# Performance work log

Measured on AMD Instinct MI355X. Metric: run time of the kernel, lower is better.

The kernel has to match this reference:

```python
import jax, jax.numpy as jnp
import numpy as np

FP8_MAX = 448.0  # torch.finfo(float8_e4m3fn).max
BLK = 128
EPS = 1e-12

def fp8_round(x):
    # saturated cast to float8_e4m3fn and back (emulates to_fp8_saturated)
    y = jnp.clip(x, -FP8_MAX, FP8_MAX)
    return y.astype(jnp.float8_e4m3fn).astype(jnp.float32)

def per_tile_quant_dequant(x):
    # activation: 1x128 tiles along the feature dim
    S, D = x.shape
    t = x.reshape(S, D // BLK, BLK)
    amax = jnp.max(jnp.abs(t), axis=-1, keepdims=True)
    scale = jnp.maximum(amax, EPS) / FP8_MAX
    q = fp8_round(t / scale)
    return (q * scale).reshape(S, D)

def per_block_quant_dequant_weight(w):
    # weight: 128x128 blocks, w is [ne, dout, din]
    ne, do, di = w.shape
    blk = w.reshape(ne, do // BLK, BLK, di // BLK, BLK)
    amax = jnp.max(jnp.abs(blk), axis=(2, 4), keepdims=True)
    scale = jnp.maximum(amax, EPS) / FP8_MAX
    q = fp8_round(blk / scale)
    return (q * scale).reshape(ne, do, di)

def setup_inputs() -> dict:
    key = jax.random.key(0)
    k1, k2 = jax.random.split(key)
    NE, DOUT, DIN, SEQ = 8, 1024, 2048, 16384
    x = jax.random.normal(k1, (SEQ, DIN), dtype=jnp.float32)
    w = jax.random.normal(k2, (NE * DOUT, DIN), dtype=jnp.float32) * 0.02
    tokens_per_expert = jnp.full((NE,), SEQ // NE, dtype=jnp.int32)
    return {"input": x, "tokens_per_expert": tokens_per_expert, "weight": w}

def reference(input, tokens_per_expert, weight):
    NE = tokens_per_expert.shape[0]
    S, DIN = input.shape
    DOUT = weight.shape[0] // NE
    w = weight.reshape(NE, DOUT, DIN)
    w_dq = per_block_quant_dequant_weight(w)   # fp8 per-block weight, dequantized
    x_dq = per_tile_quant_dequant(input)       # fp8 per-tile activation, dequantized
    # grouped varlen GEMM; tokens are split equally across experts here
    T = S // NE
    xe = x_dq.reshape(NE, T, DIN)
    out = jnp.einsum('etd,eod->eto', xe, w_dq)  # [ne, T, dout]
    return out.reshape(S, DOUT)
```

## Files before the change

### kernel.cpp

```cpp
#include <hip/hip_runtime.h>
#include <hip/hip_bf16.h>
#include <hip/hip_fp8.h>

#define SEQ   16384
#define DIN_  2048
#define DOUT_ 1024
#define NE_   8
#define TPE   (SEQ / NE_)
#define NT    (DIN_ / 64)

typedef __bf16 bf16x8 __attribute__((ext_vector_type(8)));
typedef __bf16 bf16x4 __attribute__((ext_vector_type(4)));
typedef float  f32x4  __attribute__((ext_vector_type(4)));

#define GLD(gp, lp) __builtin_amdgcn_global_load_lds( \
    (const __attribute__((address_space(1))) unsigned int*)(gp), \
    (__attribute__((address_space(3))) unsigned int*)(lp), 16, 0, 0)

__device__ __forceinline__ float fp8_round_dq_m(float v, float sinv, float s) {
    float r = v * sinv;
    r = fminf(fmaxf(r, -448.0f), 448.0f);
    __hip_fp8_e4m3 q(r);
    return (float)q * s;
}

__global__ __launch_bounds__(256) void quant_x_kernel(const float* __restrict__ X,
                                                      __bf16* __restrict__ Xq) {
    const int t    = threadIdx.x;
    const int lane = t & 63;
    const int wave = t >> 6;
    const int tile = wave * 4 + (lane >> 4);
    const int sub  = lane & 15;
    const size_t off = (size_t)tile * 128 + sub * 8;

    const int row0 = blockIdx.x * 4;
    float4 v0[4], v1[4];
    float mx[4];
    #pragma unroll
    for (int r = 0; r < 4; ++r) {
        const float* p = X + (size_t)(row0 + r) * DIN_ + off;
        v0[r] = *(const float4*)p;
        v1[r] = *(const float4*)(p + 4);
        mx[r] = fmaxf(fmaxf(fmaxf(fabsf(v0[r].x), fabsf(v0[r].y)),
                            fmaxf(fabsf(v0[r].z), fabsf(v0[r].w))),
                      fmaxf(fmaxf(fabsf(v1[r].x), fabsf(v1[r].y)),
                            fmaxf(fabsf(v1[r].z), fabsf(v1[r].w))));
    }
    #pragma unroll
    for (int o = 1; o < 16; o <<= 1) {
        #pragma unroll
        for (int r = 0; r < 4; ++r)
            mx[r] = fmaxf(mx[r], __shfl_xor(mx[r], o, 64));
    }
    #pragma unroll
    for (int r = 0; r < 4; ++r) {
        const float s    = fmaxf(mx[r], 1e-12f) / 448.0f;
        const float sinv = 1.0f / s;
        bf16x8 o;
        o[0] = (__bf16)fp8_round_dq_m(v0[r].x, sinv, s);
        o[1] = (__bf16)fp8_round_dq_m(v0[r].y, sinv, s);
        o[2] = (__bf16)fp8_round_dq_m(v0[r].z, sinv, s);
        o[3] = (__bf16)fp8_round_dq_m(v0[r].w, sinv, s);
        o[4] = (__bf16)fp8_round_dq_m(v1[r].x, sinv, s);
        o[5] = (__bf16)fp8_round_dq_m(v1[r].y, sinv, s);
        o[6] = (__bf16)fp8_round_dq_m(v1[r].z, sinv, s);
        o[7] = (__bf16)fp8_round_dq_m(v1[r].w, sinv, s);
        *(bf16x8*)(Xq + (size_t)(row0 + r) * DIN_ + off) = o;
    }
}

__global__ __launch_bounds__(256) void quant_w_kernel(const float* __restrict__ W,
                                                      __bf16* __restrict__ Wq) {
    const int rb = blockIdx.x >> 4;
    const int cb = blockIdx.x & 15;
    const int t  = threadIdx.x;

    const float* base = W + (size_t)(rb * 128) * DIN_ + cb * 128;
    const int r0 = t >> 5;
    const int c0 = (t & 31) * 4;

    float4 v[16];
    float m = 0.0f;
    #pragma unroll
    for (int i = 0; i < 16; ++i) {
        v[i] = *(const float4*)(base + (size_t)(i * 8 + r0) * DIN_ + c0);
        m = fmaxf(m, fmaxf(fmaxf(fabsf(v[i].x), fabsf(v[i].y)),
                           fmaxf(fabsf(v[i].z), fabsf(v[i].w))));
    }
    #pragma unroll
    for (int off = 1; off < 64; off <<= 1)
        m = fmaxf(m, __shfl_xor(m, off, 64));
    __shared__ float smx[4];
    if ((t & 63) == 0) smx[t >> 6] = m;
    __syncthreads();
    const float amax = fmaxf(fmaxf(smx[0], smx[1]), fmaxf(smx[2], smx[3]));
    const float s    = fmaxf(amax, 1e-12f) / 448.0f;
    const float sinv = 1.0f / s;

    __bf16* obase = Wq + (size_t)(rb * 128) * DIN_ + cb * 128;
    #pragma unroll
    for (int i = 0; i < 16; ++i) {
        bf16x4 o;
        o[0] = (__bf16)fp8_round_dq_m(v[i].x, sinv, s);
        o[1] = (__bf16)fp8_round_dq_m(v[i].y, sinv, s);
        o[2] = (__bf16)fp8_round_dq_m(v[i].z, sinv, s);
        o[3] = (__bf16)fp8_round_dq_m(v[i].w, sinv, s);
        *(bf16x4*)(obase + (size_t)(i * 8 + r0) * DIN_ + c0) = o;
    }
}

__global__ __launch_bounds__(512, 2) void gemm_kernel(const __bf16* __restrict__ X,
                                                      const __bf16* __restrict__ W,
                                                      float* __restrict__ out) {
    __shared__ __align__(16) unsigned char lds[131072];

    const int bid  = blockIdx.x;
    const int wgid = (bid & 7) * 32 + (bid >> 3);
    const int e    = wgid >> 5;
    const int tile = wgid & 31;
    const int brow = tile >> 2;
    const int bcol = tile & 3;

    const int t     = threadIdx.x;
    const int lane  = t & 63;
    const int wave  = t >> 6;
    const int wm    = wave >> 2;
    const int wn    = wave & 3;
    const int flane = lane & 15;

    const __bf16* Xt = X + (size_t)(e * TPE + brow * 256) * DIN_;
    const __bf16* Wt = W + (size_t)(e * DOUT_ + bcol * 256) * DIN_;

    auto stage = [&](int j, bool isA) {
        if (j >= NT) return;
        const unsigned base = (isA ? 0u : 65536u) + (unsigned)(j & 1) * 32768u;
        const __bf16* src = isA ? Xt : Wt;
        #pragma unroll
        for (int i = 0; i < 4; ++i) {
            const unsigned p = (unsigned)i * 8192u + (unsigned)t * 16u;
            const unsigned q = p ^ (((p >> 7) & 7u) << 4);
            GLD(src + (size_t)(q >> 7) * DIN_ + j * 64 + ((q & 127u) >> 1),
                &lds[base + p]);
        }
    };

    auto ldf = [&](unsigned base, int row, int kh) -> bf16x8 {
        unsigned p = (unsigned)row * 128u + (unsigned)kh * 64u + (unsigned)(lane >> 4) * 16u;
        p ^= ((p >> 7) & 7u) << 4;
        return *(const bf16x8*)&lds[base + p];
    };

    bf16x8 aA[4], aB[4], b0[4], b1[4];
    f32x4 acc[8][4] = {};

    #define ABASE(buf) ((unsigned)(buf) * 32768u)
    #define BBASE(buf) (65536u + (unsigned)(buf) * 32768u)
    #define PRE_A(dst, buf, kh, m0) \
        { _Pragma("unroll") for (int m_ = 0; m_ < 4; ++m_) \
            dst[m_] = ldf(ABASE(buf), wm * 128 + ((m0) + m_) * 16 + flane, kh); }
    #define PRE_B(dst, buf, kh) \
        { _Pragma("unroll") for (int n_ = 0; n_ < 4; ++n_) \
            dst[n_] = ldf(BBASE(buf), wn * 64 + n_ * 16 + flane, kh); }
    #define MFMA4x4(alo, aset, bset) \
        { _Pragma("unroll") for (int m_ = 0; m_ < 4; ++m_) \
            _Pragma("unroll") for (int n_ = 0; n_ < 4; ++n_) \
                acc[(alo) + m_][n_] = __builtin_amdgcn_mfma_f32_16x16x32_bf16( \
                    aset[m_], bset[n_], acc[(alo) + m_][n_], 0, 0, 0); }
    #define LGKM(n) \
        asm volatile("s_waitcnt lgkmcnt(" #n ")" ::: "memory"); \
        __builtin_amdgcn_sched_barrier(0);

    stage(0, false); stage(0, true); stage(1, false); stage(1, true);
    asm volatile("s_waitcnt vmcnt(8)" ::: "memory");
    __builtin_amdgcn_s_barrier();

    for (int kt = 0; kt < NT; ++kt) {
        const int buf = kt & 1;

        PRE_A(aA, buf, 0, 0);
        PRE_B(b0, buf, 0);

        PRE_A(aB, buf, 0, 4);
        LGKM(4)
        __builtin_amdgcn_s_setprio(1);
        MFMA4x4(0, aA, b0);
        __builtin_amdgcn_s_setprio(0);

        PRE_A(aA, buf, 1, 0);
        PRE_B(b1, buf, 1);
        LGKM(8)
        __builtin_amdgcn_s_setprio(1);
        MFMA4x4(4, aB, b0);
        __builtin_amdgcn_s_setprio(0);

        PRE_A(aB, buf, 1, 4);
        LGKM(4)
        __builtin_amdgcn_s_setprio(1);
        MFMA4x4(0, aA, b1);
        __builtin_amdgcn_s_setprio(0);

        LGKM(0)
        __builtin_amdgcn_s_setprio(1);
        MFMA4x4(4, aB, b1);
        __builtin_amdgcn_s_setprio(0);

        __builtin_amdgcn_s_barrier();
        stage(kt + 2, false);
        stage(kt + 2, true);
        if (kt < NT - 2) asm volatile("s_waitcnt vmcnt(8)" ::: "memory");
        else             asm volatile("s_waitcnt vmcnt(0)" ::: "memory");
        __builtin_amdgcn_s_barrier();
    }

    const int orow0 = e * TPE + brow * 256 + wm * 128;
    const int ocol0 = bcol * 256 + wn * 64;
    const int rl = (lane >> 4) * 4;
    const int cl = lane & 15;
    #pragma unroll
    for (int m = 0; m < 8; ++m)
        #pragma unroll
        for (int n = 0; n < 4; ++n)
            #pragma unroll
            for (int j = 0; j < 4; ++j) {
                const int r = orow0 + m * 16 + rl + j;
                const int c = ocol0 + n * 16 + cl;
                out[(size_t)r * DOUT_ + c] = acc[m][n][j];
            }
}

extern "C" void kernel_launch(void* const* d_in, const int* in_sizes, int n_in,
                              void* d_out, int out_size, void* d_ws, size_t ws_size,
                              hipStream_t stream) {
    const float* x = (const float*)d_in[0];
    const float* w = (const float*)d_in[2];
    float* out = (float*)d_out;

    __bf16* xq = (__bf16*)d_ws;
    __bf16* wq = (__bf16*)((char*)d_ws + (size_t)SEQ * DIN_ * sizeof(__bf16));

    quant_x_kernel<<<SEQ / 4, 256, 0, stream>>>(x, xq);
    quant_w_kernel<<<(NE_ * DOUT_ / 128) * (DIN_ / 128), 256, 0, stream>>>(w, wq);
    gemm_kernel<<<NE_ * (TPE / 256) * (DOUT_ / 256), 512, 0, stream>>>(xq, wq, out);
}
```

Baseline: 128.1 us.

## Shrink GEMM tile to 128x128 with 4 waves and cross-iteration fragment prefetch

Reduces the GEMM workgroup tile from 256x256 with 8 waves to 128x128 with 4 waves, halving LDS use to 64KB and quadrupling the grid to 1024 workgroups. Each wave now computes 64x64 instead of 128x64. The inner loop is restructured so the next k-tile's first fragments are loaded from LDS after the barrier, overlapping them with the following iteration. This aims for better occupancy and load balance across CUs, at the cost of lower arithmetic intensity and more global/L2 traffic per FLOP.

```diff
diff --git a/kernel.cpp b/kernel.cpp
--- a/kernel.cpp
+++ b/kernel.cpp
@@ -109,115 +109,101 @@
     }
 }
 
-__global__ __launch_bounds__(512, 2) void gemm_kernel(const __bf16* __restrict__ X,
+__global__ __launch_bounds__(256, 2) void gemm_kernel(const __bf16* __restrict__ X,
                                                       const __bf16* __restrict__ W,
                                                       float* __restrict__ out) {
-    __shared__ __align__(16) unsigned char lds[131072];
+    __shared__ __align__(16) unsigned char lds[65536];
 
     const int bid  = blockIdx.x;
-    const int wgid = (bid & 7) * 32 + (bid >> 3);
-    const int e    = wgid >> 5;
-    const int tile = wgid & 31;
-    const int brow = tile >> 2;
-    const int bcol = tile & 3;
+    const int wgid = (bid & 7) * 128 + (bid >> 3);
+    const int e    = wgid >> 7;
+    const int rem  = wgid & 127;
+    const int brow = rem >> 3;
+    const int bcol = rem & 7;
 
     const int t     = threadIdx.x;
     const int lane  = t & 63;
     const int wave  = t >> 6;
-    const int wm    = wave >> 2;
-    const int wn    = wave & 3;
+    const int wm    = wave >> 1;
+    const int wn    = wave & 1;
     const int flane = lane & 15;
 
-    const __bf16* Xt = X + (size_t)(e * TPE + brow * 256) * DIN_;
-    const __bf16* Wt = W + (size_t)(e * DOUT_ + bcol * 256) * DIN_;
-
-    auto stage = [&](int j, bool isA) {
+    const __bf16* Xt = X + (size_t)(e * TPE + brow * 128) * DIN_;
+    const __bf16* Wt = W + (size_t)(e * DOUT_ + bcol * 128) * DIN_;
+
+    auto stage = [&](int j) {
         if (j >= NT) return;
-        const unsigned base = (isA ? 0u : 65536u) + (unsigned)(j & 1) * 32768u;
-        const __bf16* src = isA ? Xt : Wt;
+        const unsigned ab = (unsigned)(j & 1) * 16384u;
         #pragma unroll
         for (int i = 0; i < 4; ++i) {
-            const unsigned p = (unsigned)i * 8192u + (unsigned)t * 16u;
+            const unsigned p = (unsigned)i * 4096u + (unsigned)t * 16u;
             const unsigned q = p ^ (((p >> 7) & 7u) << 4);
-            GLD(src + (size_t)(q >> 7) * DIN_ + j * 64 + ((q & 127u) >> 1),
-                &lds[base + p]);
+            GLD(Xt + (size_t)(q >> 7) * DIN_ + j * 64 + ((q & 127u) >> 1), &lds[ab + p]);
+        }
+        #pragma unroll
+        for (int i = 0; i < 4; ++i) {
+            const unsigned p = (unsigned)i * 4096u + (unsigned)t * 16u;
+            const unsigned q = p ^ (((p >> 7) & 7u) << 4);
+            GLD(Wt + (size_t)(q >> 7) * DIN_ + j * 64 + ((q & 127u) >> 1),
+                &lds[32768u + ab + p]);
         }
     };
 
-    auto ldf = [&](unsigned base, int row, int kh) -> bf16x8 {
-        unsigned p = (unsigned)row * 128u + (unsigned)kh * 64u + (unsigned)(lane >> 4) * 16u;
+    auto ldf = [&](unsigned base, int row, int ks) -> bf16x8 {
+        unsigned p = (unsigned)row * 128u + (unsigned)ks * 64u + (unsigned)(lane >> 4) * 16u;
         p ^= ((p >> 7) & 7u) << 4;
         return *(const bf16x8*)&lds[base + p];
     };
 
-    bf16x8 aA[4], aB[4], b0[4], b1[4];
-    f32x4 acc[8][4] = {};
-
-    #define ABASE(buf) ((unsigned)(buf) * 32768u)
-    #define BBASE(buf) (65536u + (unsigned)(buf) * 32768u)
-    #define PRE_A(dst, buf, kh, m0) \
+    bf16x8 a0[4], a1[4], b0[4], b1[4];
+    f32x4 acc[4][4] = {};
+
+    #define PRE8(adst, bdst, buf, ks) \
         { _Pragma("unroll") for (int m_ = 0; m_ < 4; ++m_) \
-            dst[m_] = ldf(ABASE(buf), wm * 128 + ((m0) + m_) * 16 + flane, kh); }
-    #define PRE_B(dst, buf, kh) \
-        { _Pragma("unroll") for (int n_ = 0; n_ < 4; ++n_) \
-            dst[n_] = ldf(BBASE(buf), wn * 64 + n_ * 16 + flane, kh); }
-    #define MFMA4x4(alo, aset, bset) \
+            adst[m_] = ldf((unsigned)(buf) * 16384u, wm * 64 + m_ * 16 + flane, ks); \
+          _Pragma("unroll") for (int n_ = 0; n_ < 4; ++n_) \
+            bdst[n_] = ldf(32768u + (unsigned)(buf) * 16384u, wn * 64 + n_ * 16 + flane, ks); }
+    #define MFMA16(aset, bset) \
         { _Pragma("unroll") for (int m_ = 0; m_ < 4; ++m_) \
             _Pragma("unroll") for (int n_ = 0; n_ < 4; ++n_) \
-                acc[(alo) + m_][n_] = __builtin_amdgcn_mfma_f32_16x16x32_bf16( \
-                    aset[m_], bset[n_], acc[(alo) + m_][n_], 0, 0, 0); }
-    #define LGKM(n) \
-        asm volatile("s_waitcnt lgkmcnt(" #n ")" ::: "memory"); \
-        __builtin_amdgcn_sched_barrier(0);
-
-    stage(0, false); stage(0, true); stage(1, false); stage(1, true);
+                acc[m_][n_] = __builtin_amdgcn_mfma_f32_16x16x32_bf16( \
+                    aset[m_], bset[n_], acc[m_][n_], 0, 0, 0); }
+
+    stage(0); stage(1);
     asm volatile("s_waitcnt vmcnt(8)" ::: "memory");
     __builtin_amdgcn_s_barrier();
+    PRE8(a0, b0, 0, 0);
 
     for (int kt = 0; kt < NT; ++kt) {
         const int buf = kt & 1;
 
-        PRE_A(aA, buf, 0, 0);
-        PRE_B(b0, buf, 0);
-
-        PRE_A(aB, buf, 0, 4);
-        LGKM(4)
+        PRE8(a1, b1, buf, 1);
+        asm volatile("s_waitcnt lgkmcnt(8)" ::: "memory");
+        __builtin_amdgcn_sched_barrier(0);
         __builtin_amdgcn_s_setprio(1);
-        MFMA4x4(0, aA, b0);
+        MFMA16(a0, b0);
         __builtin_amdgcn_s_setprio(0);
 
-        PRE_A(aA, buf, 1, 0);
-        PRE_B(b1, buf, 1);
-        LGKM(8)
+        asm volatile("s_waitcnt lgkmcnt(0)" ::: "memory");
+        __builtin_amdgcn_sched_barrier(0);
         __builtin_amdgcn_s_setprio(1);
-        MFMA4x4(4, aB, b0);
+        MFMA16(a1, b1);
         __builtin_amdgcn_s_setprio(0);
 
-        PRE_A(aB, buf, 1, 4);
-        LGKM(4)
-        __builtin_amdgcn_s_setprio(1);
-        MFMA4x4(0, aA, b1);
-        __builtin_amdgcn_s_setprio(0);
-
-        LGKM(0)
-        __builtin_amdgcn_s_setprio(1);
-        MFMA4x4(4, aB, b1);
-        __builtin_amdgcn_s_setprio(0);
-
         __builtin_amdgcn_s_barrier();
-        stage(kt + 2, false);
-        stage(kt + 2, true);
+        stage(kt + 2);
         if (kt < NT - 2) asm volatile("s_waitcnt vmcnt(8)" ::: "memory");
         else             asm volatile("s_waitcnt vmcnt(0)" ::: "memory");
         __builtin_amdgcn_s_barrier();
-    }
-
-    const int orow0 = e * TPE + brow * 256 + wm * 128;
-    const int ocol0 = bcol * 256 + wn * 64;
+        if (kt < NT - 1) PRE8(a0, b0, buf ^ 1, 0);
+    }
+
+    const int orow0 = e * TPE + brow * 128 + wm * 64;
+    const int ocol0 = bcol * 128 + wn * 64;
     const int rl = (lane >> 4) * 4;
     const int cl = lane & 15;
     #pragma unroll
-    for (int m = 0; m < 8; ++m)
+    for (int m = 0; m < 4; ++m)
         #pragma unroll
         for (int n = 0; n < 4; ++n)
             #pragma unroll
@@ -240,5 +226,5 @@
 
     quant_x_kernel<<<SEQ / 4, 256, 0, stream>>>(x, xq);
     quant_w_kernel<<<(NE_ * DOUT_ / 128) * (DIN_ / 128), 256, 0, stream>>>(w, wq);
-    gemm_kernel<<<NE_ * (TPE / 256) * (DOUT_ / 256), 512, 0, stream>>>(xq, wq, out);
-}
+    gemm_kernel<<<NE_ * (TPE / 128) * (DOUT_ / 128), 256, 0, stream>>>(xq, wq, out);
+}
```

Measured after the change: 123.9 us. 1.03x faster.
